# Kernel tuning notes

Measured on AMD Instinct MI355X. Metric: run time of the kernel, lower is better.

## Reference

```python
import jax, jax.numpy as jnp
import numpy as np

N = 250000   # atoms
E = 500000   # directed bond edges
B = 10000    # molecules
IN = 39      # atom feature dim (in_channels)
H = 128      # hidden_channels
ED = 10      # edge_dim
NUM_TIMESTEPS = 2


def setup_inputs() -> dict:
    key = jax.random.key(0)
    ks = iter(jax.random.split(key, 40))
    p = lambda shape: jax.random.normal(next(ks), shape, dtype=jnp.float32) * 0.05
    inp = {}
    inp["x"] = jax.random.normal(next(ks), (N, IN), dtype=jnp.float32)
    inp["edge_attr"] = jax.random.normal(next(ks), (E, ED), dtype=jnp.float32)
    # lin1
    inp["W_lin1"] = p((H, IN)); inp["b_lin1"] = p((H,))
    # GATEConv
    inp["gate_W1"] = p((H, H + ED)); inp["gate_W2"] = p((H, H))
    inp["gate_att_l"] = p((H,)); inp["gate_att_r"] = p((H,)); inp["gate_bias"] = p((H,))
    # GRUCell after GATEConv
    inp["gru1_Wih"] = p((3 * H, H)); inp["gru1_Whh"] = p((3 * H, H))
    inp["gru1_bih"] = p((3 * H,)); inp["gru1_bhh"] = p((3 * H,))
    # atom GATConv (num_layers-1 == 1)
    inp["conv_W"] = p((H, H)); inp["conv_att_src"] = p((H,)); inp["conv_att_dst"] = p((H,)); inp["conv_bias"] = p((H,))
    inp["gru2_Wih"] = p((3 * H, H)); inp["gru2_Whh"] = p((3 * H, H))
    inp["gru2_bih"] = p((3 * H,)); inp["gru2_bhh"] = p((3 * H,))
    # mol GATConv (bipartite atoms -> molecules, shared lin)
    inp["mol_W"] = p((H, H)); inp["mol_att_src"] = p((H,)); inp["mol_att_dst"] = p((H,)); inp["mol_bias"] = p((H,))
    inp["grum_Wih"] = p((3 * H, H)); inp["grum_Whh"] = p((3 * H, H))
    inp["grum_bih"] = p((3 * H,)); inp["grum_bhh"] = p((3 * H,))
    # lin2 + head
    inp["W_lin2"] = p((H, H)); inp["b_lin2"] = p((H,))
    inp["W_head"] = p((1, H)); inp["b_head"] = p((1,))
    inp["edge_index"] = jax.random.randint(next(ks), (2, E), 0, N, dtype=jnp.int32)
    inp["batch"] = jnp.sort(jax.random.randint(next(ks), (N,), 0, B, dtype=jnp.int32))
    return inp


def _gru(xg, hg, Wih, Whh, bih, bhh):
    # torch.nn.GRUCell semantics
    gi = xg @ Wih.T + bih
    gh = hg @ Whh.T + bhh
    ir, iz, inn = jnp.split(gi, 3, axis=-1)
    hr, hz, hn = jnp.split(gh, 3, axis=-1)
    r = jax.nn.sigmoid(ir + hr)
    z = jax.nn.sigmoid(iz + hz)
    n = jnp.tanh(inn + r * hn)
    return (1.0 - z) * n + z * hg


def _seg_softmax(logits, seg, num):
    # PyG softmax over target-index segments (stable, +1e-16 denom)
    m = jax.ops.segment_max(logits, seg, num_segments=num)
    e = jnp.exp(logits - m[seg])
    s = jax.ops.segment_sum(e, seg, num_segments=num)
    return e / (s[seg] + 1e-16)


def reference(x, edge_attr, W_lin1, b_lin1, gate_W1, gate_W2, gate_att_l, gate_att_r, gate_bias,
              gru1_Wih, gru1_Whh, gru1_bih, gru1_bhh,
              conv_W, conv_att_src, conv_att_dst, conv_bias,
              gru2_Wih, gru2_Whh, gru2_bih, gru2_bhh,
              mol_W, mol_att_src, mol_att_dst, mol_bias,
              grum_Wih, grum_Whh, grum_bih, grum_bhh,
              W_lin2, b_lin2, W_head, b_head,
              edge_index, batch):
    lrelu = lambda v: jax.nn.leaky_relu(v, 0.01)
    src, dst = edge_index[0], edge_index[1]  # (j, i): messages flow j -> i
    # initial atom embedding
    x = lrelu(x @ W_lin1.T + b_lin1)
    # ---- GATEConv (edge-attr-aware attention, aggr='add') ----
    xj = x[src]                                                   # [E, H]
    he = lrelu(jnp.concatenate([xj, edge_attr], axis=-1) @ gate_W1.T)
    alpha = lrelu(he @ gate_att_l + x[dst] @ gate_att_r)          # [E]
    alpha = _seg_softmax(alpha, dst, N)
    h = jax.ops.segment_sum((xj @ gate_W2.T) * alpha[:, None], dst, num_segments=N) + gate_bias
    h = jax.nn.elu(h)
    x = jax.nn.relu(_gru(h, x, gru1_Wih, gru1_Whh, gru1_bih, gru1_bhh))
    # ---- atom GATConv (heads=1, neg_slope=0.01, no self loops) ----
    xl = x @ conv_W.T
    a = lrelu((xl * conv_att_src).sum(-1)[src] + (xl * conv_att_dst).sum(-1)[dst])
    a = _seg_softmax(a, dst, N)
    h = jax.ops.segment_sum(xl[src] * a[:, None], dst, num_segments=N) + conv_bias
    h = jax.nn.relu(h)
    x = jax.nn.relu(_gru(h, x, gru2_Wih, gru2_Whh, gru2_bih, gru2_bhh))
    # ---- attentive graph readout: bipartite GAT atoms -> molecules ----
    out = jax.nn.relu(jax.ops.segment_sum(x, batch, num_segments=B))  # [B, H]
    for _ in range(NUM_TIMESTEPS):
        xs = x @ mol_W.T                                          # src transform [N, H]
        od = out @ mol_W.T                                        # dst transform [B, H]
        a = lrelu((xs * mol_att_src).sum(-1) + ((od * mol_att_dst).sum(-1))[batch])
        a = _seg_softmax(a, batch, B)
        h = jax.ops.segment_sum(xs * a[:, None], batch, num_segments=B) + mol_bias
        h = jax.nn.elu(h)
        out = jax.nn.relu(_gru(h, out, grum_Wih, grum_Whh, grum_bih, grum_bhh))
    out = out @ W_lin2.T + b_lin2
    out = out @ W_head.T + b_head                                 # [B, 1]
    return out.squeeze(-1)                                        # [B]
```

## Files before the change

### kernel.cpp

```cpp
#include <hip/hip_runtime.h>
#include <hip/hip_bf16.h>
#include <type_traits>

typedef __hip_bfloat16 bf16;

constexpr int N_  = 250000;
constexpr int E_  = 500000;
constexpr int B_  = 10000;
constexpr int H_  = 128;

typedef short s8v __attribute__((ext_vector_type(8)));
typedef float f4v __attribute__((ext_vector_type(4)));

__device__ __forceinline__ float b2f(bf16 v){ return __bfloat162float(v); }
__device__ __forceinline__ bf16  f2b(float v){ return __float2bfloat16(v); }
__device__ __forceinline__ float lrelu_f(float v){ return v > 0.f ? v : 0.01f*v; }
__device__ __forceinline__ float sigmoid_f(float x){ return __builtin_amdgcn_rcpf(1.f+__expf(-x)); }
__device__ __forceinline__ float tanh_f(float x){ return 1.f - 2.f*__builtin_amdgcn_rcpf(__expf(2.f*x)+1.f); }
__device__ __forceinline__ float elu_f(float v){ return v > 0.f ? v : __expf(v)-1.f; }
__device__ __forceinline__ unsigned f2b_bits(float f){
  bf16 h=__float2bfloat16(f); unsigned short s; __builtin_memcpy(&s,&h,2); return (unsigned)s;
}
__device__ __forceinline__ void unp8(uint4 v, float* o){
  o[0]=__uint_as_float(v.x<<16); o[1]=__uint_as_float(v.x&0xffff0000u);
  o[2]=__uint_as_float(v.y<<16); o[3]=__uint_as_float(v.y&0xffff0000u);
  o[4]=__uint_as_float(v.z<<16); o[5]=__uint_as_float(v.z&0xffff0000u);
  o[6]=__uint_as_float(v.w<<16); o[7]=__uint_as_float(v.w&0xffff0000u);
}

struct W2B { const float* s; bf16* d; int rows, ld, ow, cw; };
struct W2B11 { W2B seg[11]; };
__global__ void w2ball_k(W2B11 p){
  W2B g=p.seg[blockIdx.y];
  int i=blockIdx.x*256+threadIdx.x;
  if (i>=g.rows*g.ow) return;
  int r=i/g.ow, k=i-r*g.ow;
  g.d[i] = f2b(k<g.cw ? g.s[(size_t)r*g.ld+k] : 0.f);
}

__global__ __launch_bounds__(256) void lin1_mfma_k(const float* __restrict__ X0, const bf16* __restrict__ Wb,
                            const float* __restrict__ bias, const float* __restrict__ dvec,
                            bf16* __restrict__ Y, float* __restrict__ dout, int M){
  __shared__ __align__(16) bf16 sx[64][72];
  __shared__ float sdot[4][64];
  int wv=threadIdx.x>>6, lane=threadIdx.x&63;
  int n=lane&15, q=lane>>4;
  int c0=wv*32;
  s8v wB[2][2];
  #pragma unroll
  for (int ct=0;ct<2;ct++)
    #pragma unroll
    for (int kk=0;kk<2;kk++)
      wB[ct][kk]=*(const s8v*)(Wb+(size_t)(c0+ct*16+n)*64+kk*32+q*8);
  float bb[2];
  #pragma unroll
  for (int ct=0;ct<2;ct++) bb[ct]=bias[c0+ct*16+n];
  float va[2]={dvec[c0+n], dvec[c0+16+n]};
  for (int i=threadIdx.x;i<64*25;i+=256){ int r=i/25,k=39+(i-(i/25)*25); sx[r][k]=f2b(0.f); }
  for (long r0=(long)blockIdx.x*64; r0<M; r0+=(long)gridDim.x*64){
    __syncthreads();
    for (int f=threadIdx.x; f<64*39; f+=256){
      int r=f/39, k=f-(f/39)*39; long row=r0+r;
      sx[r][k]= f2b(row<M ? X0[row*39+k] : 0.f);
    }
    __syncthreads();
    s8v a[4][2];
    #pragma unroll
    for (int rt=0;rt<4;rt++)
      #pragma unroll
      for (int kk=0;kk<2;kk++)
        a[rt][kk]=*(const s8v*)&sx[rt*16+n][kk*32+q*8];
    f4v acc[4][2];
    #pragma unroll
    for (int rt=0;rt<4;rt++)
      #pragma unroll
      for (int ct=0;ct<2;ct++) acc[rt][ct]=(f4v){0.f,0.f,0.f,0.f};
    #pragma unroll
    for (int kk=0;kk<2;kk++)
      #pragma unroll
      for (int rt=0;rt<4;rt++)
        #pragma unroll
        for (int ct=0;ct<2;ct++)
          acc[rt][ct]=__builtin_amdgcn_mfma_f32_16x16x32_bf16(a[rt][kk],wB[ct][kk],acc[rt][ct],0,0,0);
    #pragma unroll
    for (int rt=0;rt<4;rt++){
      #pragma unroll
      for (int rg=0;rg<4;rg++){
        float y0=lrelu_f(acc[rt][0][rg]+bb[0]);
        float y1=lrelu_f(acc[rt][1][rg]+bb[1]);
        long row=r0+rt*16+q*4+rg;
        if (row<M){
          Y[row*128+c0+n]   =f2b(y0);
          Y[row*128+c0+16+n]=f2b(y1);
        }
        float pa=y0*va[0]+y1*va[1];
        #pragma unroll
        for (int o=1;o<16;o<<=1) pa+=__shfl_xor(pa,o);
        if (n==0) sdot[wv][rt*16+q*4+rg]=pa;
      }
    }
    __syncthreads();
    if (threadIdx.x<64){
      long row=r0+threadIdx.x;
      if (row<M) dout[row]=sdot[0][threadIdx.x]+sdot[1][threadIdx.x]+sdot[2][threadIdx.x]+sdot[3][threadIdx.x];
    }
  }
}

template<int ACT,int NDOT>
__global__ __launch_bounds__(256) void lin_mfma_k(const bf16* __restrict__ X, const bf16* __restrict__ Wb,
                            const float* __restrict__ bias, bf16* __restrict__ Y,
                            const float* __restrict__ v1, const float* __restrict__ v2,
                            float* __restrict__ d1, float* __restrict__ d2, int M){
  __shared__ float sdot[2][4][64];
  int wv=threadIdx.x>>6, lane=threadIdx.x&63;
  int n=lane&15, q=lane>>4;
  int c0=wv*32;
  s8v wB[2][4];
  #pragma unroll
  for (int ct=0;ct<2;ct++)
    #pragma unroll
    for (int kk=0;kk<4;kk++)
      wB[ct][kk]=*(const s8v*)(Wb+(size_t)(c0+ct*16+n)*128+kk*32+q*8);
  float bb[2];
  #pragma unroll
  for (int ct=0;ct<2;ct++) bb[ct]=bias? bias[c0+ct*16+n]:0.f;
  float va[2][2];
  if constexpr (NDOT>=1){ va[0][0]=v1[c0+n]; va[0][1]=v1[c0+16+n]; }
  if constexpr (NDOT>=2){ va[1][0]=v2[c0+n]; va[1][1]=v2[c0+16+n]; }
  for (long r0=(long)blockIdx.x*64; r0<M; r0+=(long)gridDim.x*64){
    s8v a[4][4];
    #pragma unroll
    for (int rt=0;rt<4;rt++){
      long row=r0+rt*16+n; if (row>=M) row=M-1;
      #pragma unroll
      for (int kk=0;kk<4;kk++) a[rt][kk]=*(const s8v*)(X+row*128+kk*32+q*8);
    }
    f4v acc[4][2];
    #pragma unroll
    for (int rt=0;rt<4;rt++)
      #pragma unroll
      for (int ct=0;ct<2;ct++) acc[rt][ct]=(f4v){0.f,0.f,0.f,0.f};
    #pragma unroll
    for (int kk=0;kk<4;kk++)
      #pragma unroll
      for (int rt=0;rt<4;rt++)
        #pragma unroll
        for (int ct=0;ct<2;ct++)
          acc[rt][ct]=__builtin_amdgcn_mfma_f32_16x16x32_bf16(a[rt][kk],wB[ct][kk],acc[rt][ct],0,0,0);
    #pragma unroll
    for (int rt=0;rt<4;rt++){
      #pragma unroll
      for (int rg=0;rg<4;rg++){
        float y0=acc[rt][0][rg]+bb[0];
        float y1=acc[rt][1][rg]+bb[1];
        if (ACT==2){ y0=elu_f(y0); y1=elu_f(y1); }
        long row=r0+rt*16+q*4+rg;
        if (row<M){
          Y[row*128+c0+n]   =f2b(y0);
          Y[row*128+c0+16+n]=f2b(y1);
        }
        if constexpr (NDOT>=1){
          float pa=y0*va[0][0]+y1*va[0][1];
          float pb=0.f;
          if constexpr (NDOT>=2) pb=y0*va[1][0]+y1*va[1][1];
          #pragma unroll
          for (int o=1;o<16;o<<=1){
            pa+=__shfl_xor(pa,o);
            if constexpr (NDOT>=2) pb+=__shfl_xor(pb,o);
          }
          if (n==0){
            sdot[0][wv][rt*16+q*4+rg]=pa;
            if constexpr (NDOT>=2) sdot[1][wv][rt*16+q*4+rg]=pb;
          }
        }
      }
    }
    if constexpr (NDOT>=1){
      __syncthreads();
      if (threadIdx.x<64){
        long row=r0+threadIdx.x;
        if (row<M){
          d1[row]=sdot[0][0][threadIdx.x]+sdot[0][1][threadIdx.x]+sdot[0][2][threadIdx.x]+sdot[0][3][threadIdx.x];
          if constexpr (NDOT>=2)
            d2[row]=sdot[1][0][threadIdx.x]+sdot[1][1][threadIdx.x]+sdot[1][2][threadIdx.x]+sdot[1][3][threadIdx.x];
        }
      }
      __syncthreads();
    }
  }
}

__global__ __launch_bounds__(512,1) void gru_mfma_k(const bf16* __restrict__ A, const bf16* __restrict__ X,
                            const bf16* __restrict__ Wih, const bf16* __restrict__ Whh,
                            const float* __restrict__ bih, const float* __restrict__ bhh,
                            bf16* __restrict__ dest, int M){
  __shared__ __align__(16) bf16 sA[2][32][136];
  __shared__ __align__(16) bf16 sX[2][32][136];
  int wv=threadIdx.x>>6, lane=threadIdx.x&63;
  int n=lane&15, q=lane>>4;
  int c0=wv*16;
  s8v wI[3][4], wH[3][4];
  #pragma unroll
  for (int g=0;g<3;g++)
    #pragma unroll
    for (int kk=0;kk<4;kk++){
      size_t off=((size_t)(g*128+c0+n))*128+kk*32+q*8;
      wI[g][kk]=*(const s8v*)(Wih+off);
      wH[g][kk]=*(const s8v*)(Whh+off);
    }
  int col=c0+n;
  float br =bih[col]+bhh[col];
  float bz =bih[128+col]+bhh[128+col];
  float bni=bih[256+col], bnh=bhh[256+col];

  int srow=wv*4+q;
  int schunk=n;
  long step=(long)gridDim.x*32;
  long r0=(long)blockIdx.x*32;
  int buf=0;
  {
    long rowg=r0+srow; if (rowg>=M) rowg=M-1;
    uint4 va=*(const uint4*)(A+rowg*128+schunk*8);
    uint4 vx=*(const uint4*)(X+rowg*128+schunk*8);
    *(uint4*)&sA[0][srow][schunk*8]=va;
    *(uint4*)&sX[0][srow][schunk*8]=vx;
  }
  __syncthreads();
  for (; r0<M; r0+=step){
    long rn=r0+step;
    uint4 va, vx; bool pre = rn<M;
    if (pre){
      long rowg=rn+srow; if (rowg>=M) rowg=M-1;
      va=*(const uint4*)(A+rowg*128+schunk*8);
      vx=*(const uint4*)(X+rowg*128+schunk*8);
    }
    f4v acc[6][2];
    #pragma unroll
    for (int g=0;g<6;g++)
      #pragma unroll
      for (int rt=0;rt<2;rt++) acc[g][rt]=(f4v){0.f,0.f,0.f,0.f};
    #pragma unroll
    for (int kk=0;kk<4;kk++){
      s8v aA[2], aX[2];
      #pragma unroll
      for (int rt=0;rt<2;rt++){
        aA[rt]=*(const s8v*)&sA[buf][rt*16+n][(kk*4+q)*8];
        aX[rt]=*(const s8v*)&sX[buf][rt*16+n][(kk*4+q)*8];
      }
      #pragma unroll
      for (int g=0;g<3;g++)
        #pragma unroll
        for (int rt=0;rt<2;rt++){
          acc[g  ][rt]=__builtin_amdgcn_mfma_f32_16x16x32_bf16(aA[rt],wI[g][kk],acc[g  ][rt],0,0,0);
          acc[3+g][rt]=__builtin_amdgcn_mfma_f32_16x16x32_bf16(aX[rt],wH[g][kk],acc[3+g][rt],0,0,0);
        }
    }
    float xv[2][4];
    #pragma unroll
    for (int rt=0;rt<2;rt++)
      #pragma unroll
      for (int rg=0;rg<4;rg++)
        xv[rt][rg]=b2f(sX[buf][rt*16+q*4+rg][col]);
    #pragma unroll
    for (int rt=0;rt<2;rt++){
      #pragma unroll
      for (int rg=0;rg<4;rg++){
        long row=r0+rt*16+q*4+rg;
        if (row<M){
          float rgate=sigmoid_f(acc[0][rt][rg]+acc[3][rt][rg]+br);
          float zgate=sigmoid_f(acc[1][rt][rg]+acc[4][rt][rg]+bz);
          float nn=tanh_f(acc[2][rt][rg]+bni + rgate*(acc[5][rt][rg]+bnh));
          float o=(1.f-zgate)*nn + zgate*xv[rt][rg];
          dest[row*128+col]=f2b(fmaxf(o,0.f));
        }
      }
    }
    if (pre){
      *(uint4*)&sA[buf^1][srow][schunk*8]=va;
      *(uint4*)&sX[buf^1][srow][schunk*8]=vx;
    }
    __syncthreads();
    buf^=1;
  }
}

__global__ __launch_bounds__(512,1) void gru_mol_mfma_k(const float* __restrict__ A, const float* __restrict__ X,
                            const bf16* __restrict__ Wih, const bf16* __restrict__ Whh,
                            const float* __restrict__ bih, const float* __restrict__ bhh,
                            float* __restrict__ dest, int M){
  __shared__ __align__(16) bf16 sA[32][136];
  __shared__ __align__(16) bf16 sX[32][136];
  int wv=threadIdx.x>>6, lane=threadIdx.x&63;
  int n=lane&15, q=lane>>4;
  int c0=wv*16;
  s8v wI[3][4], wH[3][4];
  #pragma unroll
  for (int g=0;g<3;g++)
    #pragma unroll
    for (int kk=0;kk<4;kk++){
      size_t off=((size_t)(g*128+c0+n))*128+kk*32+q*8;
      wI[g][kk]=*(const s8v*)(Wih+off);
      wH[g][kk]=*(const s8v*)(Whh+off);
    }
  int col=c0+n;
  float br =bih[col]+bhh[col];
  float bz =bih[128+col]+bhh[128+col];
  float bni=bih[256+col], bnh=bhh[256+col];

  long r0=(long)blockIdx.x*32;
  {
    int t=threadIdx.x; int row=t>>4, ch=t&15;
    long rowg=r0+row;
    float4 a1,a2,x1,x2;
    if (rowg<M){
      a1=*(const float4*)(A+rowg*128+ch*8); a2=*(const float4*)(A+rowg*128+ch*8+4);
      x1=*(const float4*)(X+rowg*128+ch*8); x2=*(const float4*)(X+rowg*128+ch*8+4);
    } else {
      a1=a2=x1=x2=make_float4(0,0,0,0);
    }
    uint4 pa, px;
    pa.x=f2b_bits(a1.x)|(f2b_bits(a1.y)<<16); pa.y=f2b_bits(a1.z)|(f2b_bits(a1.w)<<16);
    pa.z=f2b_bits(a2.x)|(f2b_bits(a2.y)<<16); pa.w=f2b_bits(a2.z)|(f2b_bits(a2.w)<<16);
    px.x=f2b_bits(x1.x)|(f2b_bits(x1.y)<<16); px.y=f2b_bits(x1.z)|(f2b_bits(x1.w)<<16);
    px.z=f2b_bits(x2.x)|(f2b_bits(x2.y)<<16); px.w=f2b_bits(x2.z)|(f2b_bits(x2.w)<<16);
    *(uint4*)&sA[row][ch*8]=pa;
    *(uint4*)&sX[row][ch*8]=px;
  }
  __syncthreads();
  f4v acc[6][2];
  #pragma unroll
  for (int g=0;g<6;g++)
    #pragma unroll
    for (int rt=0;rt<2;rt++) acc[g][rt]=(f4v){0.f,0.f,0.f,0.f};
  #pragma unroll
  for (int kk=0;kk<4;kk++){
    s8v aA[2], aX[2];
    #pragma unroll
    for (int rt=0;rt<2;rt++){
      aA[rt]=*(const s8v*)&sA[rt*16+n][(kk*4+q)*8];
      aX[rt]=*(const s8v*)&sX[rt*16+n][(kk*4+q)*8];
    }
    #pragma unroll
    for (int g=0;g<3;g++)
      #pragma unroll
      for (int rt=0;rt<2;rt++){
        acc[g  ][rt]=__builtin_amdgcn_mfma_f32_16x16x32_bf16(aA[rt],wI[g][kk],acc[g  ][rt],0,0,0);
        acc[3+g][rt]=__builtin_amdgcn_mfma_f32_16x16x32_bf16(aX[rt],wH[g][kk],acc[3+g][rt],0,0,0);
      }
  }
  #pragma unroll
  for (int rt=0;rt<2;rt++){
    #pragma unroll
    for (int rg=0;rg<4;rg++){
      long row=r0+rt*16+q*4+rg;
      if (row<M){
        float xv=X[row*128+col];
        float rgate=sigmoid_f(acc[0][rt][rg]+acc[3][rt][rg]+br);
        float zgate=sigmoid_f(acc[1][rt][rg]+acc[4][rt][rg]+bz);
        float nn=tanh_f(acc[2][rt][rg]+bni + rgate*(acc[5][rt][rg]+bnh));
        float o=(1.f-zgate)*nn + zgate*xv;
        dest[row*128+col]=fmaxf(o,0.f);
      }
    }
  }
}

__global__ __launch_bounds__(256) void gate_edge_logits_k(const bf16* __restrict__ u, const float* __restrict__ ea,
                                   const float* __restrict__ gW1, const float* __restrict__ att_l,
                                   const float* __restrict__ ddst, const int* __restrict__ src,
                                   const int* __restrict__ dst, const int* __restrict__ epos,
                                   float* __restrict__ elog, int E){
  int wv=threadIdx.x>>6, lane=threadIdx.x&63;
  int t=lane&31;
  float w[10][4];
  #pragma unroll
  for (int k=0;k<10;k++)
    #pragma unroll
    for (int j=0;j<4;j++)
      w[k][j]=gW1[(size_t)(t*4+j)*138 + 128 + k];
  float al[4];
  #pragma unroll
  for (int j=0;j<4;j++) al[j]=att_l[t*4+j];

  long stride=(long)gridDim.x*8;
  long e=(long)blockIdx.x*8 + wv*2 + (lane>>5);
  if (e>=E) return;
  int sj=src[e];
  uint2 uv=*(const uint2*)(u+(size_t)sj*128+t*4);
  const float2* er=(const float2*)(ea+(size_t)e*10);
  float2 c0=er[0],c1=er[1],c2=er[2],c3=er[3],c4=er[4];
  float dv=ddst[dst[e]];
  int ep=epos[e];
  while (true){
    long en=e+stride; bool has=en<E;
    uint2 uvn=make_uint2(0,0);
    float2 d0={0,0},d1={0,0},d2={0,0},d3={0,0},d4={0,0};
    float dvn=0.f; int epn=0;
    if (has){
      int sjn=src[en];
      uvn=*(const uint2*)(u+(size_t)sjn*128+t*4);
      const float2* ern=(const float2*)(ea+(size_t)en*10);
      d0=ern[0];d1=ern[1];d2=ern[2];d3=ern[3];d4=ern[4];
      dvn=ddst[dst[en]];
      epn=epos[en];
    }
    float uf[4];
    uf[0]=__uint_as_float(uv.x<<16); uf[1]=__uint_as_float(uv.x&0xffff0000u);
    uf[2]=__uint_as_float(uv.y<<16); uf[3]=__uint_as_float(uv.y&0xffff0000u);
    float acc=0.f;
    #pragma unroll
    for (int j=0;j<4;j++){
      float v=uf[j];
      v+=c0.x*w[0][j]; v+=c0.y*w[1][j];
      v+=c1.x*w[2][j]; v+=c1.y*w[3][j];
      v+=c2.x*w[4][j]; v+=c2.y*w[5][j];
      v+=c3.x*w[6][j]; v+=c3.y*w[7][j];
      v+=c4.x*w[8][j]; v+=c4.y*w[9][j];
      acc+=lrelu_f(v)*al[j];
    }
    #pragma unroll
    for (int o=16;o;o>>=1) acc+=__shfl_xor(acc,o);
    if (t==0) elog[ep]=lrelu_f(acc+dv);
    if (!has) break;
    e=en; uv=uvn; c0=d0;c1=d1;c2=d2;c3=d3;c4=d4; dv=dvn; ep=epn;
  }
}

template<int ACT>
__global__ void node_gather_k(const float* __restrict__ elog, const int* __restrict__ srcp,
                              const int* __restrict__ ptr, const bf16* __restrict__ V,
                              const float* __restrict__ bias, bf16* __restrict__ S, int M){
  int wv=threadIdx.x>>6, lane=threadIdx.x&63;
  int g=lane>>3, t=lane&7;
  int node=blockIdx.x*32 + wv*8 + g;
  if (node>=M) return;
  int p0=ptr[node], p1=ptr[node+1];
  float m=-INFINITY;
  for (int p=p0+t;p<p1;p+=8) m=fmaxf(m,elog[p]);
  #pragma unroll
  for (int o=4;o;o>>=1) m=fmaxf(m,__shfl_xor(m,o));
  float ssum=0.f;
  float acc[16]={0,0,0,0,0,0,0,0,0,0,0,0,0,0,0,0};
  if (p0<p1){
    float lg=elog[p0];
    const uint4* vp=(const uint4*)(V+(size_t)srcp[p0]*128+t*16);
    uint4 va=vp[0], vb=vp[1];
    for (int p=p0+1;p<p1;p++){
      float lgn=elog[p];
      const uint4* vpn=(const uint4*)(V+(size_t)srcp[p]*128+t*16);
      uint4 van=vpn[0], vbn=vpn[1];
      float e=__expf(lg-m); ssum+=e;
      float xf[8]; unp8(va,xf);
      #pragma unroll
      for (int j=0;j<8;j++) acc[j]+=e*xf[j];
      unp8(vb,xf);
      #pragma unroll
      for (int j=0;j<8;j++) acc[8+j]+=e*xf[j];
      lg=lgn; va=van; vb=vbn;
    }
    float e=__expf(lg-m); ssum+=e;
    float xf[8]; unp8(va,xf);
    #pragma unroll
    for (int j=0;j<8;j++) acc[j]+=e*xf[j];
    unp8(vb,xf);
    #pragma unroll
    for (int j=0;j<8;j++) acc[8+j]+=e*xf[j];
  }
  float inv=1.f/(ssum+1e-16f);
  #pragma unroll
  for (int j=0;j<16;j++) acc[j]*=inv;
  if (ACT==1){
    #pragma unroll
    for (int j=0;j<16;j++) acc[j]=fmaxf(acc[j]+bias[t*16+j],0.f);
  }
  uint4 o1,o2;
  o1.x=f2b_bits(acc[0])|(f2b_bits(acc[1])<<16);
  o1.y=f2b_bits(acc[2])|(f2b_bits(acc[3])<<16);
  o1.z=f2b_bits(acc[4])|(f2b_bits(acc[5])<<16);
  o1.w=f2b_bits(acc[6])|(f2b_bits(acc[7])<<16);
  o2.x=f2b_bits(acc[8])|(f2b_bits(acc[9])<<16);
  o2.y=f2b_bits(acc[10])|(f2b_bits(acc[11])<<16);
  o2.z=f2b_bits(acc[12])|(f2b_bits(acc[13])<<16);
  o2.w=f2b_bits(acc[14])|(f2b_bits(acc[15])<<16);
  *(uint4*)(S+(size_t)node*128+t*16)=o1;
  *(uint4*)(S+(size_t)node*128+t*16+8)=o2;
}

__global__ __launch_bounds__(256) void conv_gather_k(const float* __restrict__ dsrc, const float* __restrict__ ddst,
    const int* __restrict__ ptr, const int* __restrict__ srcp,
    const bf16* __restrict__ V, const float* __restrict__ bias, bf16* __restrict__ S, int M){
  int wv=threadIdx.x>>6, lane=threadIdx.x&63;
  int g=lane>>3, t=lane&7;
  int node=blockIdx.x*32 + wv*8 + g;
  if (node>=M) return;
  int p0=ptr[node], p1=ptr[node+1];
  float dvn=ddst[node];
  float m=-INFINITY, s=0.f;
  float acc[16]={0,0,0,0,0,0,0,0,0,0,0,0,0,0,0,0};
  if (p0<p1){
    int sj=srcp[p0];
    float ls=dsrc[sj];
    const uint4* vp=(const uint4*)(V+(size_t)sj*128+t*16);
    uint4 va=vp[0], vb=vp[1];
    for (int p=p0+1;p<p1;p++){
      int sjn=srcp[p];
      float lsn=dsrc[sjn];
      const uint4* vpn=(const uint4*)(V+(size_t)sjn*128+t*16);
      uint4 van=vpn[0], vbn=vpn[1];
      float l=lrelu_f(ls+dvn);
      float mn=fmaxf(m,l), sc=__expf(m-mn), ee=__expf(l-mn);
      float xf[8]; unp8(va,xf);
      s=s*sc+ee;
      #pragma unroll
      for (int j=0;j<8;j++) acc[j]=acc[j]*sc+ee*xf[j];
      unp8(vb,xf);
      #pragma unroll
      for (int j=0;j<8;j++) acc[8+j]=acc[8+j]*sc+ee*xf[j];
      m=mn; ls=lsn; va=van; vb=vbn;
    }
    float l=lrelu_f(ls+dvn);
    float mn=fmaxf(m,l), sc=__expf(m-mn), ee=__expf(l-mn);
    float xf[8]; unp8(va,xf);
    s=s*sc+ee;
    #pragma unroll
    for (int j=0;j<8;j++) acc[j]=acc[j]*sc+ee*xf[j];
    unp8(vb,xf);
    #pragma unroll
    for (int j=0;j<8;j++) acc[8+j]=acc[8+j]*sc+ee*xf[j];
  }
  float inv=1.f/(s+1e-16f);
  float r[16];
  #pragma unroll
  for (int j=0;j<16;j++) r[j]=fmaxf(acc[j]*inv+bias[t*16+j],0.f);
  uint4 o1,o2;
  o1.x=f2b_bits(r[0])|(f2b_bits(r[1])<<16);
  o1.y=f2b_bits(r[2])|(f2b_bits(r[3])<<16);
  o1.z=f2b_bits(r[4])|(f2b_bits(r[5])<<16);
  o1.w=f2b_bits(r[6])|(f2b_bits(r[7])<<16);
  o2.x=f2b_bits(r[8])|(f2b_bits(r[9])<<16);
  o2.y=f2b_bits(r[10])|(f2b_bits(r[11])<<16);
  o2.z=f2b_bits(r[12])|(f2b_bits(r[13])<<16);
  o2.w=f2b_bits(r[14])|(f2b_bits(r[15])<<16);
  *(uint4*)(S+(size_t)node*128+t*16)=o1;
  *(uint4*)(S+(size_t)node*128+t*16+8)=o2;
}

__global__ void mol_ptr_k(const int* __restrict__ batch, int* __restrict__ mptr, int n, int Bn){
  int b=blockIdx.x*256+threadIdx.x; if (b>Bn) return;
  if (b==Bn){ mptr[Bn]=n; return; }
  int lo=0, hi=n;
  while (lo<hi){ int mid=(lo+hi)>>1; if (batch[mid]<b) lo=mid+1; else hi=mid; }
  mptr[b]=lo;
}

__global__ void mol_sum_k(const bf16* __restrict__ x, const int* __restrict__ mptr,
                          float* __restrict__ out, int Bn){
  int wv=threadIdx.x>>6, lane=threadIdx.x&63;
  int b=blockIdx.x*4+wv; if (b>=Bn) return;
  int p0=mptr[b], p1=mptr[b+1];
  float a0=0.f,a1=0.f;
  for (int i=p0;i<p1;i++){ a0+=b2f(x[(size_t)i*128+lane]); a1+=b2f(x[(size_t)i*128+64+lane]); }
  out[(size_t)b*128+lane]=fmaxf(a0,0.f); out[(size_t)b*128+64+lane]=fmaxf(a1,0.f);
}

__global__ void fold_att_k(const float* __restrict__ W, const float* __restrict__ att,
                           float* __restrict__ wdd){
  int k=threadIdx.x; float a=0.f;
  for (int c=0;c<128;c++) a+=att[c]*W[(size_t)c*128+k];
  wdd[k]=a;
}

__global__ __launch_bounds__(256) void mol_fused_k(const float* __restrict__ dsrc, const int* __restrict__ mptr,
    const bf16* __restrict__ xs, const float* __restrict__ wdd, const float* __restrict__ outc,
    const float* __restrict__ bias, float* __restrict__ hb, int Bn){
  int wv=threadIdx.x>>6, lane=threadIdx.x&63;
  long b=(long)blockIdx.x*4+wv; if (b>=Bn) return;
  int p0=mptr[b], p1=mptr[b+1];
  float dd=outc[(size_t)b*128+lane]*wdd[lane]+outc[(size_t)b*128+64+lane]*wdd[64+lane];
  #pragma unroll
  for (int o=32;o;o>>=1) dd+=__shfl_xor(dd,o);
  float m=-INFINITY, s=0.f, a0=0.f, a1=0.f;
  for (int i=p0;i<p1;i++){
    float a=lrelu_f(dsrc[i]+dd);
    float x0=b2f(xs[(size_t)i*128+lane]), x1=b2f(xs[(size_t)i*128+64+lane]);
    float mn=fmaxf(m,a), sc=__expf(m-mn), ee=__expf(a-mn);
    s=s*sc+ee; a0=a0*sc+ee*x0; a1=a1*sc+ee*x1; m=mn;
  }
  float inv=1.f/(s+1e-16f);
  hb[(size_t)b*128+lane]=elu_f(a0*inv+bias[lane]);
  hb[(size_t)b*128+64+lane]=elu_f(a1*inv+bias[64+lane]);
}

__global__ void fold_head_k(const float* __restrict__ W2, const float* __restrict__ b2,
                            const float* __restrict__ Wh, const float* __restrict__ bh,
                            float* __restrict__ v){
  __shared__ float sred[128];
  int k=threadIdx.x;
  float a=0.f;
  for (int c=0;c<128;c++) a+=Wh[c]*W2[(size_t)c*128+k];
  v[k]=a;
  sred[k]=b2[k]*Wh[k]; __syncthreads();
  for (int o=64;o;o>>=1){ if (k<o) sred[k]+=sred[k+o]; __syncthreads(); }
  if (k==0) v[128]=sred[0]+bh[0];
}

__global__ void head_dot_k(const float* __restrict__ out, const float* __restrict__ v,
                           float* __restrict__ y, int M){
  __shared__ float sv[129];
  if (threadIdx.x<129) sv[threadIdx.x]=v[threadIdx.x];
  __syncthreads();
  int wv=threadIdx.x>>6, lane=threadIdx.x&63;
  long row=(long)blockIdx.x*4+wv;
  if (row>=M) return;
  float a=out[row*128+lane]*sv[lane]+out[row*128+64+lane]*sv[64+lane];
  #pragma unroll
  for (int o=32;o;o>>=1) a+=__shfl_xor(a,o);
  if (!lane) y[row]=a+sv[128];
}

__global__ void zero_i32_k(int* p, int n){ int i=blockIdx.x*256+threadIdx.x; if (i<n) p[i]=0; }
__global__ void hist_k(const int* __restrict__ dst, int* __restrict__ deg, int n){
  int e=blockIdx.x*256+threadIdx.x; if (e<n) atomicAdd(&deg[dst[e]],1);
}
__global__ void scan1_k(const int* __restrict__ deg, int* __restrict__ ptr,
                        int* __restrict__ part, int n){
  __shared__ int sd[256];
  int base=blockIdx.x*1024, tid=threadIdx.x;
  int v[4]; int ssum=0;
  #pragma unroll
  for (int j=0;j<4;j++){ int idx=base+tid*4+j; v[j]= idx<n? deg[idx]:0; ssum+=v[j]; }
  sd[tid]=ssum; __syncthreads();
  for (int o=1;o<256;o<<=1){ int t = tid>=o? sd[tid-o]:0; __syncthreads(); sd[tid]+=t; __syncthreads(); }
  int excl=sd[tid]-ssum;
  #pragma unroll
  for (int j=0;j<4;j++){ int idx=base+tid*4+j; if (idx<n) ptr[idx]=excl; excl+=v[j]; }
  if (tid==255) part[blockIdx.x]=sd[255];
}
__global__ void scan2_k(int* part, int nb){
  __shared__ int sd[512];
  int tid=threadIdx.x;
  int v= tid<nb? part[tid]:0; sd[tid]=v; __syncthreads();
  for (int o=1;o<512;o<<=1){ int t = tid>=o? sd[tid-o]:0; __syncthreads(); sd[tid]+=t; __syncthreads(); }
  if (tid<nb) part[tid]=sd[tid]-v;
}
__global__ void scan3_k(int* __restrict__ ptr, const int* __restrict__ part,
                        int* __restrict__ wofs, int n, int total){
  int i=blockIdx.x*256+threadIdx.x;
  if (i<n){ int val=ptr[i]+part[i>>10]; ptr[i]=val; wofs[i]=val; }
  if (i==0) ptr[n]=total;
}
__global__ void fill_csr_k(const int* __restrict__ dst, const int* __restrict__ src,
                           int* __restrict__ wofs, int* __restrict__ srcp,
                           int* __restrict__ epos, int n){
  int e=blockIdx.x*256+threadIdx.x;
  if (e<n){ int p=atomicAdd(&wofs[dst[e]],1); srcp[p]=src[e]; epos[e]=p; }
}

extern "C" void kernel_launch(void* const* d_in, const int* in_sizes, int n_in,
                              void* d_out, int out_size, void* d_ws, size_t ws_size,
                              hipStream_t stream){
  (void)in_sizes; (void)n_in; (void)out_size; (void)ws_size;
  const float* x0        =(const float*)d_in[0];
  const float* edge_attr =(const float*)d_in[1];
  const float* W_lin1    =(const float*)d_in[2];
  const float* b_lin1    =(const float*)d_in[3];
  const float* gate_W1   =(const float*)d_in[4];
  const float* gate_W2   =(const float*)d_in[5];
  const float* gate_att_l=(const float*)d_in[6];
  const float* gate_att_r=(const float*)d_in[7];
  const float* gate_bias =(const float*)d_in[8];
  const float* g1_Wih=(const float*)d_in[9];  const float* g1_Whh=(const float*)d_in[10];
  const float* g1_bih=(const float*)d_in[11]; const float* g1_bhh=(const float*)d_in[12];
  const float* conv_W=(const float*)d_in[13];
  const float* conv_att_src=(const float*)d_in[14];
  const float* conv_att_dst=(const float*)d_in[15];
  const float* conv_bias   =(const float*)d_in[16];
  const float* g2_Wih=(const float*)d_in[17]; const float* g2_Whh=(const float*)d_in[18];
  const float* g2_bih=(const float*)d_in[19]; const float* g2_bhh=(const float*)d_in[20];
  const float* mol_W=(const float*)d_in[21];
  const float* mol_att_src=(const float*)d_in[22];
  const float* mol_att_dst=(const float*)d_in[23];
  const float* mol_bias   =(const float*)d_in[24];
  const float* gm_Wih=(const float*)d_in[25]; const float* gm_Whh=(const float*)d_in[26];
  const float* gm_bih=(const float*)d_in[27]; const float* gm_bhh=(const float*)d_in[28];
  const float* W_lin2=(const float*)d_in[29]; const float* b_lin2=(const float*)d_in[30];
  const float* W_head=(const float*)d_in[31]; const float* b_head=(const float*)d_in[32];
  const int* ei   =(const int*)d_in[33];
  const int* batch=(const int*)d_in[34];
  const int* src=ei; const int* dst=ei+E_;
  float* y=(float*)d_out;

  const size_t NH=(size_t)N_*H_, BH=(size_t)B_*H_;
  bf16* b0  =(bf16*)d_ws;
  bf16* b1  =b0+NH;
  bf16* b2v =b1+NH;
  float* outA=(float*)(b2v+NH);
  float* outB=outA+BH;
  float* hb  =outB+BH;
  float* elog=hb+BH;
  float* dsrc=elog+E_;
  float* ddst=dsrc+N_;
  float* alog=ddst+N_;
  float* wdd =alog+N_;
  float* dd  =wdd+128;
  int* deg =(int*)(dd+B_);
  int* ptr =deg+N_;
  int* wofs=ptr+N_+1;
  int* part=wofs+N_;
  int* mptr=part+512;
  int* srcp=mptr+B_+1;
  int* epos=srcp+E_;
  uintptr_t wbase=((uintptr_t)(epos+E_)+255)&~(uintptr_t)255;
  bf16* wb_gw1 =(bf16*)wbase;
  bf16* wb_gw2 =wb_gw1 +128*128;
  bf16* wb_conv=wb_gw2 +128*128;
  bf16* wb_mol =wb_conv+128*128;
  bf16* wb_g1i =wb_mol +128*128;
  bf16* wb_g1h =wb_g1i +384*128;
  bf16* wb_g2i =wb_g1h +384*128;
  bf16* wb_g2h =wb_g2i +384*128;
  bf16* wb_l1  =wb_g2h +384*128;
  bf16* wb_gmi =wb_l1  +128*64;
  bf16* wb_gmh =wb_gmi +384*128;

  W2B11 wp;
  wp.seg[0]={gate_W1,wb_gw1,128,138,128,128};
  wp.seg[1]={gate_W2,wb_gw2,128,128,128,128};
  wp.seg[2]={conv_W ,wb_conv,128,128,128,128};
  wp.seg[3]={mol_W  ,wb_mol ,128,128,128,128};
  wp.seg[4]={g1_Wih,wb_g1i,384,128,128,128};
  wp.seg[5]={g1_Whh,wb_g1h,384,128,128,128};
  wp.seg[6]={g2_Wih,wb_g2i,384,128,128,128};
  wp.seg[7]={g2_Whh,wb_g2h,384,128,128,128};
  wp.seg[8]={W_lin1,wb_l1 ,128, 39, 64, 39};
  wp.seg[9]={gm_Wih,wb_gmi,384,128,128,128};
  wp.seg[10]={gm_Whh,wb_gmh,384,128,128,128};
  w2ball_k<<<dim3(192,11),256,0,stream>>>(wp);

  zero_i32_k<<<(N_+255)/256,256,0,stream>>>(deg,N_);
  hist_k<<<(E_+255)/256,256,0,stream>>>(dst,deg,E_);
  int nb=(N_+1023)/1024;
  scan1_k<<<nb,256,0,stream>>>(deg,ptr,part,N_);
  scan2_k<<<1,512,0,stream>>>(part,nb);
  scan3_k<<<(N_+255)/256,256,0,stream>>>(ptr,part,wofs,N_,E_);
  fill_csr_k<<<(E_+255)/256,256,0,stream>>>(dst,src,wofs,srcp,epos,E_);
  mol_ptr_k<<<(B_+1+255)/256,256,0,stream>>>(batch,mptr,N_,B_);

  lin1_mfma_k<<<1024,256,0,stream>>>(x0,wb_l1,b_lin1,gate_att_r,b0,ddst,N_);

  const int GL=768, GN8=(N_+31)/32;
  lin_mfma_k<0,0><<<GL,256,0,stream>>>(b0,wb_gw1,nullptr,b1,nullptr,nullptr,nullptr,nullptr,N_);
  gate_edge_logits_k<<<8192,256,0,stream>>>(b1,edge_attr,gate_W1,gate_att_l,ddst,src,dst,epos,elog,E_);
  node_gather_k<0><<<GN8,256,0,stream>>>(elog,srcp,ptr,b0,nullptr,b2v,N_);
  lin_mfma_k<2,0><<<GL,256,0,stream>>>(b2v,wb_gw2,gate_bias,b1,nullptr,nullptr,nullptr,nullptr,N_);
  gru_mfma_k<<<1024,512,0,stream>>>(b1,b0,wb_g1i,wb_g1h,g1_bih,g1_bhh,b2v,N_);
  lin_mfma_k<0,2><<<GL,256,0,stream>>>(b2v,wb_conv,nullptr,b0,conv_att_src,conv_att_dst,dsrc,ddst,N_);
  conv_gather_k<<<GN8,256,0,stream>>>(dsrc,ddst,ptr,srcp,b0,conv_bias,b1,N_);
  gru_mfma_k<<<1024,512,0,stream>>>(b1,b2v,wb_g2i,wb_g2h,g2_bih,g2_bhh,b0,N_);
  mol_sum_k<<<(B_+3)/4,256,0,stream>>>(b0,mptr,outA,B_);
  lin_mfma_k<0,1><<<GL,256,0,stream>>>(b0,wb_mol,nullptr,b1,mol_att_src,nullptr,dsrc,nullptr,N_);
  fold_att_k<<<1,128,0,stream>>>(mol_W,mol_att_dst,wdd);
  float* out_cur=outA; float* out_nxt=outB;
  const int GB32=(B_+31)/32;
  for (int ts=0; ts<2; ts++){
    mol_fused_k<<<(B_+3)/4,256,0,stream>>>(dsrc,mptr,b1,wdd,out_cur,mol_bias,hb,B_);
    gru_mol_mfma_k<<<GB32,512,0,stream>>>(hb,out_cur,wb_gmi,wb_gmh,gm_bih,gm_bhh,out_nxt,B_);
    float* tmp=out_cur; out_cur=out_nxt; out_nxt=tmp;
  }
  fold_head_k<<<1,128,0,stream>>>(W_lin2,b_lin2,W_head,b_head,elog);
  head_dot_k<<<(B_+3)/4,256,0,stream>>>(out_cur,elog,y,B_);
}
```

Measured before the change: 911.6 us.

## Apply mol_W after softmax aggregation instead of transforming all atoms

Measured after the change: 936.1 us. 1.03x slower.

```diff
diff --git a/kernel.cpp b/kernel.cpp
--- a/kernel.cpp
+++ b/kernel.cpp
@@ -191,6 +191,20 @@
   }
 }
 
+__global__ void rowdot_k(const bf16* __restrict__ Y, const float* __restrict__ v,
+                         float* __restrict__ d, int M){
+  __shared__ float sv[128];
+  if (threadIdx.x<128) sv[threadIdx.x]=v[threadIdx.x];
+  __syncthreads();
+  int wv=threadIdx.x>>6, lane=threadIdx.x&63;
+  long row=(long)blockIdx.x*4+wv;
+  if (row>=M) return;
+  float a=b2f(Y[row*128+lane])*sv[lane]+b2f(Y[row*128+64+lane])*sv[64+lane];
+  #pragma unroll
+  for (int o=32;o;o>>=1) a+=__shfl_xor(a,o);
+  if (!lane) d[row]=a;
+}
+
 __global__ __launch_bounds__(512,1) void gru_mfma_k(const bf16* __restrict__ A, const bf16* __restrict__ X,
                             const bf16* __restrict__ Wih, const bf16* __restrict__ Whh,
                             const float* __restrict__ bih, const float* __restrict__ bhh,
@@ -564,16 +578,19 @@
   out[(size_t)b*128+lane]=fmaxf(a0,0.f); out[(size_t)b*128+64+lane]=fmaxf(a1,0.f);
 }
 
-__global__ void fold_att_k(const float* __restrict__ W, const float* __restrict__ att,
-                           float* __restrict__ wdd){
-  int k=threadIdx.x; float a=0.f;
-  for (int c=0;c<128;c++) a+=att[c]*W[(size_t)c*128+k];
-  wdd[k]=a;
-}
-
-__global__ __launch_bounds__(256) void mol_fused_k(const float* __restrict__ dsrc, const int* __restrict__ mptr,
-    const bf16* __restrict__ xs, const float* __restrict__ wdd, const float* __restrict__ outc,
-    const float* __restrict__ bias, float* __restrict__ hb, int Bn){
+__global__ void fold_att2_k(const float* __restrict__ W, const float* __restrict__ as_,
+                            const float* __restrict__ ad, float* __restrict__ wms,
+                            float* __restrict__ wdd){
+  int k=threadIdx.x;
+  const float* at = blockIdx.x? ad : as_;
+  float a=0.f;
+  for (int c=0;c<128;c++) a+=at[c]*W[(size_t)c*128+k];
+  if (blockIdx.x) wdd[k]=a; else wms[k]=a;
+}
+
+__global__ __launch_bounds__(256) void mol_fused_raw_k(const float* __restrict__ dsrc, const int* __restrict__ mptr,
+    const bf16* __restrict__ x, const float* __restrict__ wdd, const float* __restrict__ outc,
+    float* __restrict__ P, int Bn){
   int wv=threadIdx.x>>6, lane=threadIdx.x&63;
   long b=(long)blockIdx.x*4+wv; if (b>=Bn) return;
   int p0=mptr[b], p1=mptr[b+1];
@@ -583,13 +600,44 @@
   float m=-INFINITY, s=0.f, a0=0.f, a1=0.f;
   for (int i=p0;i<p1;i++){
     float a=lrelu_f(dsrc[i]+dd);
-    float x0=b2f(xs[(size_t)i*128+lane]), x1=b2f(xs[(size_t)i*128+64+lane]);
+    float x0=b2f(x[(size_t)i*128+lane]), x1=b2f(x[(size_t)i*128+64+lane]);
     float mn=fmaxf(m,a), sc=__expf(m-mn), ee=__expf(a-mn);
     s=s*sc+ee; a0=a0*sc+ee*x0; a1=a1*sc+ee*x1; m=mn;
   }
   float inv=1.f/(s+1e-16f);
-  hb[(size_t)b*128+lane]=elu_f(a0*inv+bias[lane]);
-  hb[(size_t)b*128+64+lane]=elu_f(a1*inv+bias[64+lane]);
+  P[(size_t)b*128+lane]=a0*inv;
+  P[(size_t)b*128+64+lane]=a1*inv;
+}
+
+__global__ __launch_bounds__(256) void mol_lin_k(const float* __restrict__ P, const float* __restrict__ W,
+                         const float* __restrict__ bias, float* __restrict__ hb, int Bn){
+  __shared__ bf16 sW[128][132];
+  __shared__ float sP[8][128];
+  __shared__ float sb[128];
+  for (int i=threadIdx.x;i<128*128;i+=256){ int r=i>>7,k=i&127; sW[r][k]=f2b(W[i]); }
+  if (threadIdx.x<128) sb[threadIdx.x]=bias[threadIdx.x];
+  __syncthreads();
+  int sub=threadIdx.x>>5, c0=threadIdx.x&31;
+  for (long b0=(long)blockIdx.x*8; b0<Bn; b0+=(long)gridDim.x*8){
+    __syncthreads();
+    for (int i=threadIdx.x;i<8*32;i+=256){
+      int rr=i>>5,q=i&31; long b=b0+rr;
+      *(float4*)&sP[rr][q*4] = (b<Bn)? *(const float4*)(P+b*128+q*4) : make_float4(0,0,0,0);
+    }
+    __syncthreads();
+    long b=b0+sub;
+    if (b<Bn){
+      float acc[4]={0,0,0,0};
+      #pragma unroll 4
+      for (int k=0;k<128;k++){
+        float pv=sP[sub][k];
+        #pragma unroll
+        for (int j=0;j<4;j++) acc[j]+=pv*b2f(sW[c0+32*j][k]);
+      }
+      #pragma unroll
+      for (int j=0;j<4;j++) hb[b*128+c0+32*j]=elu_f(acc[j]+sb[c0+32*j]);
+    }
+  }
 }
 
 __global__ void fold_head_k(const float* __restrict__ W2, const float* __restrict__ b2,
@@ -723,6 +771,7 @@
   bf16* wb_l1  =wb_g2h +384*128;
   bf16* wb_gmi =wb_l1  +128*64;
   bf16* wb_gmh =wb_gmi +384*128;
+  float* wms = dd;
 
   W2B11 wp;
   wp.seg[0]={gate_W1,wb_gw1,128,138,128,128};
@@ -737,6 +786,7 @@
   wp.seg[9]={gm_Wih,wb_gmi,384,128,128,128};
   wp.seg[10]={gm_Whh,wb_gmh,384,128,128,128};
   w2ball_k<<<dim3(192,11),256,0,stream>>>(wp);
+  fold_att2_k<<<2,128,0,stream>>>(mol_W,mol_att_src,mol_att_dst,wms,wdd);
 
   zero_i32_k<<<(N_+255)/256,256,0,stream>>>(deg,N_);
   hist_k<<<(E_+255)/256,256,0,stream>>>(dst,deg,E_);
@@ -749,7 +799,7 @@
 
   lin1_mfma_k<<<1024,256,0,stream>>>(x0,wb_l1,b_lin1,gate_att_r,b0,ddst,N_);
 
-  const int GL=768, GN8=(N_+31)/32;
+  const int GL=768, GN8=(N_+31)/32, GN4=(N_+3)/4;
   lin_mfma_k<0,0><<<GL,256,0,stream>>>(b0,wb_gw1,nullptr,b1,nullptr,nullptr,nullptr,nullptr,N_);
   gate_edge_logits_k<<<8192,256,0,stream>>>(b1,edge_attr,gate_W1,gate_att_l,ddst,src,dst,epos,elog,E_);
   node_gather_k<0><<<GN8,256,0,stream>>>(elog,srcp,ptr,b0,nullptr,b2v,N_);
@@ -759,12 +809,13 @@
   conv_gather_k<<<GN8,256,0,stream>>>(dsrc,ddst,ptr,srcp,b0,conv_bias,b1,N_);
   gru_mfma_k<<<1024,512,0,stream>>>(b1,b2v,wb_g2i,wb_g2h,g2_bih,g2_bhh,b0,N_);
   mol_sum_k<<<(B_+3)/4,256,0,stream>>>(b0,mptr,outA,B_);
-  lin_mfma_k<0,1><<<GL,256,0,stream>>>(b0,wb_mol,nullptr,b1,mol_att_src,nullptr,dsrc,nullptr,N_);
-  fold_att_k<<<1,128,0,stream>>>(mol_W,mol_att_dst,wdd);
+  rowdot_k<<<GN4,256,0,stream>>>(b0,wms,dsrc,N_);
   float* out_cur=outA; float* out_nxt=outB;
+  float* P=(float*)b1;
   const int GB32=(B_+31)/32;
   for (int ts=0; ts<2; ts++){
-    mol_fused_k<<<(B_+3)/4,256,0,stream>>>(dsrc,mptr,b1,wdd,out_cur,mol_bias,hb,B_);
+    mol_fused_raw_k<<<(B_+3)/4,256,0,stream>>>(dsrc,mptr,b0,wdd,out_cur,P,B_);
+    mol_lin_k<<<256,256,0,stream>>>(P,mol_W,mol_bias,hb,B_);
     gru_mol_mfma_k<<<GB32,512,0,stream>>>(hb,out_cur,wb_gmi,wb_gmh,gm_bih,gm_bhh,out_nxt,B_);
     float* tmp=out_cur; out_cur=out_nxt; out_nxt=tmp;
   }
```
